# Kernel optimization log

Measured on AMD Instinct MI355X. Metric: run time of the kernel, lower is better.

## Reference

```python
import jax, jax.numpy as jnp
import numpy as np

HIDDEN = 1024
NUM_SLOTS = 8
VOCAB = 32768
B, T = 32, 2048


def setup_inputs() -> dict:
    key = jax.random.key(0)
    k1, k2, k3 = jax.random.split(key, 3)
    hidden_states = jax.random.normal(k1, (B, T, HIDDEN), dtype=jnp.float32)
    attention_mask = jnp.ones((B, T), dtype=jnp.int32)
    # slot projector weight, torch Linear stores [out, in] = [H*num_slots, H]
    W_proj = jax.random.normal(k2, (HIDDEN * NUM_SLOTS, HIDDEN), dtype=jnp.float32) * 0.02
    codebook = jax.random.normal(k3, (VOCAB, HIDDEN), dtype=jnp.float32) * 0.02
    return {"hidden_states": hidden_states, "attention_mask": attention_mask,
            "W_proj": W_proj, "codebook": codebook}


def _masked_mean(states, mask):
    # states [B,T,H], mask [B,T] -> [B,H]
    w = mask.astype(states.dtype)
    denom = jnp.clip(w.sum(axis=1, keepdims=True), 1.0)
    return jnp.einsum('bth,bt->bh', states, w) / denom


def reference(hidden_states, attention_mask, W_proj, codebook):
    pooled = _masked_mean(hidden_states, attention_mask)          # [B,H]
    pre_q = (pooled @ W_proj.T).reshape(-1, NUM_SLOTS, HIDDEN)    # [B,S,H]
    distances = (jnp.sum(pre_q ** 2, axis=-1, keepdims=True)
                 - 2.0 * jnp.einsum('bsh,vh->bsv', pre_q, codebook)
                 + jnp.sum(codebook ** 2, axis=-1)[None, None, :])  # [B,S,V]
    logits = -distances
    indices = jnp.argmax(logits, axis=-1)                         # [B,S]
    embedded = codebook[indices]                                  # [B,S,H]
    quantized = pre_q + jax.lax.stop_gradient(embedded - pre_q)
    commitment_loss = jnp.mean((pre_q - jax.lax.stop_gradient(embedded)) ** 2)
    codebook_loss = jnp.mean((embedded - jax.lax.stop_gradient(pre_q)) ** 2)
    return logits, indices, pre_q, quantized, commitment_loss, codebook_loss
```

## Files before the change

kernel.cpp:

```cpp
#include <hip/hip_runtime.h>
#include <hip/hip_bf16.h>

#define B_ 32
#define T_ 2048
#define H_ 1024
#define S_ 8
#define V_ 32768
#define ROWS 256
#define OUTO 8192
#define NCHUNK 64
#define TCHUNK 32
#define NCB 256
#define DELTA2 0.008f
#define MAXCAND 512

typedef __attribute__((ext_vector_type(8))) short s16x8;
typedef __attribute__((ext_vector_type(8))) unsigned short u16x8;
typedef __attribute__((ext_vector_type(4))) float f32x4;

__device__ __forceinline__ unsigned short bf16hi(float x) {
  return __builtin_bit_cast(unsigned short, __float2bfloat16(x));
}

__global__ void pool_kernel(const float* __restrict__ hidden,
                            const int* __restrict__ mask,
                            float* __restrict__ part_pool,
                            int* __restrict__ cntpart) {
  int b = blockIdx.x;
  int chunk = blockIdx.y;
  int t0 = chunk * TCHUNK;
  int h4 = threadIdx.x * 4;
  const float* base = hidden + ((size_t)b * T_ + t0) * H_ + h4;
  const int* mrow = mask + (size_t)b * T_ + t0;
  float a0 = 0.f, a1 = 0.f, a2 = 0.f, a3 = 0.f;
  int mcount = 0;
#pragma unroll 4
  for (int i = 0; i < TCHUNK; ++i) {
    int mi = mrow[i];
    float m = (float)mi;
    mcount += mi;
    float4 v = *reinterpret_cast<const float4*>(base + (size_t)i * H_);
    a0 += m * v.x; a1 += m * v.y; a2 += m * v.z; a3 += m * v.w;
  }
  float* pp = part_pool + ((size_t)chunk * B_ + b) * H_ + h4;
  *reinterpret_cast<float4*>(pp) = make_float4(a0, a1, a2, a3);
  if (threadIdx.x == 0) cntpart[chunk * B_ + b] = mcount;
}

__global__ void pool_reduce_kernel(const float* __restrict__ part_pool,
                                   const int* __restrict__ cntpart,
                                   float* __restrict__ pooledT,
                                   int* __restrict__ cnt) {
  int g = blockIdx.x * 256 + threadIdx.x;
  float s = 0.f;
  for (int c = 0; c < NCHUNK; ++c) s += part_pool[(size_t)c * (H_ * B_) + g];
  int b = g >> 10, h = g & 1023;
  pooledT[h * B_ + b] = s;
  if (g < B_) {
    int cs = 0;
    for (int c = 0; c < NCHUNK; ++c) cs += cntpart[c * B_ + g];
    cnt[g] = cs;
  }
}

__global__ __launch_bounds__(256) void proj_kernel(const float* __restrict__ Wp,
                            const float* __restrict__ pooledT,
                            const int* __restrict__ cnt,
                            float* __restrict__ preq) {
  __shared__ float pl[32][516];
  const int t = threadIdx.x;
  const int og = t >> 5, b = t & 31;
  const int o0 = blockIdx.x * 32;
  float acc0 = 0.f, acc1 = 0.f, acc2 = 0.f, acc3 = 0.f;
  const float* wb = Wp + (size_t)(o0 + og * 4) * H_;
  for (int pass = 0; pass < 2; ++pass) {
    int k0 = pass * 512;
    __syncthreads();
#pragma unroll
    for (int i = 0; i < 16; ++i) {
      int f = i * 1024 + t * 4;
      int hl = f >> 5, b4 = f & 31;
      float4 v = *reinterpret_cast<const float4*>(&pooledT[(size_t)(k0 + hl) * 32 + b4]);
      pl[b4 + 0][hl] = v.x; pl[b4 + 1][hl] = v.y;
      pl[b4 + 2][hl] = v.z; pl[b4 + 3][hl] = v.w;
    }
    __syncthreads();
    const float* w0 = wb + k0;
#pragma unroll 4
    for (int j = 0; j < 128; ++j) {
      float4 p = *reinterpret_cast<const float4*>(&pl[b][4 * j]);
      float4 a = *reinterpret_cast<const float4*>(w0 + 4 * j);
      float4 c = *reinterpret_cast<const float4*>(w0 + H_ + 4 * j);
      float4 d = *reinterpret_cast<const float4*>(w0 + 2 * H_ + 4 * j);
      float4 e = *reinterpret_cast<const float4*>(w0 + 3 * H_ + 4 * j);
      acc0 += a.x * p.x + a.y * p.y + a.z * p.z + a.w * p.w;
      acc1 += c.x * p.x + c.y * p.y + c.z * p.z + c.w * p.w;
      acc2 += d.x * p.x + d.y * p.y + d.z * p.z + d.w * p.w;
      acc3 += e.x * p.x + e.y * p.y + e.z * p.z + e.w * p.w;
    }
  }
  float denom = fmaxf((float)cnt[b], 1.0f);
  size_t obase = (size_t)b * OUTO + o0 + og * 4;
  preq[obase + 0] = acc0 / denom;
  preq[obase + 1] = acc1 / denom;
  preq[obase + 2] = acc2 / denom;
  preq[obase + 3] = acc3 / denom;
}

__global__ void aprep_kernel(const float* __restrict__ preq,
                             unsigned short* __restrict__ A_img,
                             float* __restrict__ xnorm) {
  int row = blockIdx.x;
  int t = threadIdx.x;
  int k0 = 4 * t;
  int ks = k0 >> 5, kk = k0 & 31;
  float4 v = reinterpret_cast<const float4*>(preq + (size_t)row * H_)[t];
  float xv[4] = {v.x, v.y, v.z, v.w};
  unsigned short hv[4];
  float s = 0.f;
#pragma unroll
  for (int i = 0; i < 4; ++i) { s += xv[i] * xv[i]; hv[i] = bf16hi(xv[i]); }
  *reinterpret_cast<ushort4*>(&A_img[(size_t)ks * 8192 + row * 32 + kk]) =
      make_ushort4(hv[0], hv[1], hv[2], hv[3]);
#pragma unroll
  for (int off = 1; off < 64; off <<= 1) s += __shfl_xor(s, off);
  __shared__ float ps[4];
  if ((t & 63) == 0) ps[t >> 6] = s;
  __syncthreads();
  if (t == 0) xnorm[row] = ps[0] + ps[1] + ps[2] + ps[3];
}

__global__ __launch_bounds__(512, 2) void dist_kernel(
    const unsigned short* __restrict__ A_img, const float* __restrict__ codebook,
    const float* __restrict__ xnorm, float* __restrict__ logits,
    float* __restrict__ pscore) {
  __shared__ __align__(16) unsigned short Bs[2][128][40];
  __shared__ float cn[128];
  __shared__ float xns[256];
  __shared__ float bwv[2][256];

  const int t = threadIdx.x;
  const int l = t & 63;
  const int w = t >> 6;
  const int cb = w & 1;
  const int m0 = (w >> 1) * 64;
  const int lr = l & 15, lq = l >> 4;
  const int blk = blockIdx.x;
  const int v0 = blk * 128;

  if (t < 256) xns[t] = xnorm[t];

  const int sn = t >> 2;
  const int sk = (t & 3) * 8;
  const float* cbp = codebook + (size_t)(v0 + sn) * H_ + sk;
  float csq = 0.f;

  f32x4 acc[4][4];
#pragma unroll
  for (int i = 0; i < 4; ++i)
#pragma unroll
    for (int j = 0; j < 4; ++j) acc[i][j] = (f32x4){0.f, 0.f, 0.f, 0.f};

  unsigned int aoff[4];
#pragma unroll
  for (int mt = 0; mt < 4; ++mt)
    aoff[mt] = (unsigned int)((m0 + mt * 16 + lr) * 32 + lq * 8);

#define LOAD_A(DST, KS)                                                           \
  _Pragma("unroll")                                                               \
  for (int mt = 0; mt < 4; ++mt)                                                  \
    DST[mt] = *reinterpret_cast<const s16x8*>(&A_img[(size_t)(KS) * 8192 + aoff[mt]]);

#define CONV(BUF, X0, X1)                                                         \
  {                                                                               \
    float xv[8] = {X0.x, X0.y, X0.z, X0.w, X1.x, X1.y, X1.z, X1.w};               \
    u16x8 hv;                                                                     \
    _Pragma("unroll")                                                             \
    for (int i = 0; i < 8; ++i) { float x = xv[i]; csq += x * x; hv[i] = bf16hi(x); } \
    *reinterpret_cast<u16x8*>(&Bs[BUF][sn][sk]) = hv;                             \
  }

#define BAR()                                                                     \
  asm volatile("s_waitcnt lgkmcnt(0)" ::: "memory");                              \
  __builtin_amdgcn_s_barrier();                                                   \
  __builtin_amdgcn_sched_barrier(0);

#define STEP(KS, AU, AN, CC0, CC1, CL0, CL1)                                      \
  {                                                                               \
    LOAD_A(AN, (KS) + 1);                                                         \
    int kl = (KS) + 3; if (kl > 31) kl = 31;                                      \
    CL0 = *reinterpret_cast<const float4*>(cbp + kl * 32);                        \
    CL1 = *reinterpret_cast<const float4*>(cbp + kl * 32 + 4);                    \
    s16x8 bh[4];                                                                  \
    _Pragma("unroll")                                                             \
    for (int nt = 0; nt < 4; ++nt)                                                \
      bh[nt] = *reinterpret_cast<const s16x8*>(&Bs[(KS) & 1][cb * 64 + nt * 16 + lr][lq * 8]); \
    __builtin_amdgcn_s_setprio(1);                                                \
    _Pragma("unroll")                                                             \
    for (int mt = 0; mt < 4; ++mt)                                                \
      _Pragma("unroll")                                                           \
      for (int nt = 0; nt < 4; ++nt)                                              \
        acc[mt][nt] = __builtin_amdgcn_mfma_f32_16x16x32_bf16(AU[mt], bh[nt], acc[mt][nt], 0, 0, 0); \
    __builtin_amdgcn_s_setprio(0);                                                \
    CONV(((KS) + 1) & 1, CC0, CC1);                                               \
    BAR();                                                                        \
  }

  s16x8 a0[4], a1[4], a2[4];
  LOAD_A(a0, 0);
  float4 c00 = *reinterpret_cast<const float4*>(cbp);
  float4 c01 = *reinterpret_cast<const float4*>(cbp + 4);
  float4 c10 = *reinterpret_cast<const float4*>(cbp + 32);
  float4 c11 = *reinterpret_cast<const float4*>(cbp + 36);
  float4 c20 = *reinterpret_cast<const float4*>(cbp + 64);
  float4 c21 = *reinterpret_cast<const float4*>(cbp + 68);
  CONV(0, c00, c01);
  BAR();

  for (int ks = 0; ks < 30; ks += 3) {
    STEP(ks,     a0, a1, c10, c11, c00, c01);
    STEP(ks + 1, a1, a2, c20, c21, c10, c11);
    STEP(ks + 2, a2, a0, c00, c01, c20, c21);
  }
  {
    LOAD_A(a1, 31);
    s16x8 bh[4];
#pragma unroll
    for (int nt = 0; nt < 4; ++nt)
      bh[nt] = *reinterpret_cast<const s16x8*>(&Bs[0][cb * 64 + nt * 16 + lr][lq * 8]);
    __builtin_amdgcn_s_setprio(1);
#pragma unroll
    for (int mt = 0; mt < 4; ++mt)
#pragma unroll
      for (int nt = 0; nt < 4; ++nt)
        acc[mt][nt] = __builtin_amdgcn_mfma_f32_16x16x32_bf16(a0[mt], bh[nt], acc[mt][nt], 0, 0, 0);
    __builtin_amdgcn_s_setprio(0);
    CONV(1, c10, c11);
    BAR();
  }
  {
    s16x8 bh[4];
#pragma unroll
    for (int nt = 0; nt < 4; ++nt)
      bh[nt] = *reinterpret_cast<const s16x8*>(&Bs[1][cb * 64 + nt * 16 + lr][lq * 8]);
    __builtin_amdgcn_s_setprio(1);
#pragma unroll
    for (int mt = 0; mt < 4; ++mt)
#pragma unroll
      for (int nt = 0; nt < 4; ++nt)
        acc[mt][nt] = __builtin_amdgcn_mfma_f32_16x16x32_bf16(a1[mt], bh[nt], acc[mt][nt], 0, 0, 0);
    __builtin_amdgcn_s_setprio(0);
  }

  csq += __shfl_xor(csq, 1);
  csq += __shfl_xor(csq, 2);
  if ((t & 3) == 0) cn[sn] = csq;
  __syncthreads();

  const float NEG = -3.402823466e38f;
#pragma unroll
  for (int mt = 0; mt < 4; ++mt) {
#pragma unroll
    for (int r = 0; r < 4; ++r) {
      int row = m0 + mt * 16 + lq * 4 + r;
      float xn = xns[row];
      float bs = NEG;
#pragma unroll
      for (int nt = 0; nt < 4; ++nt) {
        int col = cb * 64 + nt * 16 + lr;
        float sc = 2.f * acc[mt][nt][r] - cn[col];
        logits[(size_t)row * V_ + v0 + col] = sc - xn;
        bs = fmaxf(bs, sc);
      }
#pragma unroll
      for (int off = 1; off < 16; off <<= 1) bs = fmaxf(bs, __shfl_xor(bs, off));
      if (lr == 0) bwv[cb][row] = bs;
    }
  }
  __syncthreads();
  if (t < 256) pscore[(size_t)t * NCB + blk] = fmaxf(bwv[0][t], bwv[1][t]);
}

__global__ __launch_bounds__(256) void finalize_kernel(
    const float* __restrict__ preq, const float* __restrict__ codebook,
    const float* __restrict__ logits, const float* __restrict__ xnorm,
    const float* __restrict__ pscore,
    float* __restrict__ out_idx, float* __restrict__ out_quant,
    float* __restrict__ lsum) {
  int row = blockIdx.x;
  int t = threadIdx.x;
  float m = pscore[(size_t)row * NCB + t];
#pragma unroll
  for (int off = 1; off < 64; off <<= 1) m = fmaxf(m, __shfl_xor(m, off));
  __shared__ float wm[4];
  if ((t & 63) == 0) wm[t >> 6] = m;
  __syncthreads();
  float M = fmaxf(fmaxf(wm[0], wm[1]), fmaxf(wm[2], wm[3]));
  float thr = M - xnorm[row] - DELTA2;
  __shared__ int cand[MAXCAND];
  __shared__ int ncand;
  if (t == 0) ncand = 0;
  __syncthreads();
  const float* lrow = logits + (size_t)row * V_;
#pragma unroll 4
  for (int it = 0; it < 32; ++it) {
    int c0 = it * 1024 + t * 4;
    float4 lg = *reinterpret_cast<const float4*>(lrow + c0);
    if (lg.x >= thr) { int p = atomicAdd(&ncand, 1); if (p < MAXCAND) cand[p] = c0; }
    if (lg.y >= thr) { int p = atomicAdd(&ncand, 1); if (p < MAXCAND) cand[p] = c0 + 1; }
    if (lg.z >= thr) { int p = atomicAdd(&ncand, 1); if (p < MAXCAND) cand[p] = c0 + 2; }
    if (lg.w >= thr) { int p = atomicAdd(&ncand, 1); if (p < MAXCAND) cand[p] = c0 + 3; }
  }
  __syncthreads();
  int total = ncand;
  const float* pr = preq + (size_t)row * H_;
  int idx;
  if (total <= MAXCAND) {
    __shared__ double sd[4];
    double best = -1.0e300; int bi = V_;
    for (int j = 0; j < total; ++j) {
      int c = cand[j];
      const float* cr = codebook + (size_t)c * H_;
      float4 cv = reinterpret_cast<const float4*>(cr)[t];
      float4 pv = reinterpret_cast<const float4*>(pr)[t];
      double p = (double)cv.x * (2.0 * (double)pv.x - (double)cv.x)
               + (double)cv.y * (2.0 * (double)pv.y - (double)cv.y)
               + (double)cv.z * (2.0 * (double)pv.z - (double)cv.z)
               + (double)cv.w * (2.0 * (double)pv.w - (double)cv.w);
#pragma unroll
      for (int off = 1; off < 64; off <<= 1) p += __shfl_xor(p, off);
      if ((t & 63) == 0) sd[t >> 6] = p;
      __syncthreads();
      double s = sd[0] + sd[1] + sd[2] + sd[3];
      if (s > best || (s == best && c < bi)) { best = s; bi = c; }
      __syncthreads();
    }
    idx = bi;
  } else {
    double best = -1.0e300; int bi = V_;
    for (int c = t; c < V_; c += 256) {
      const float* cr = codebook + (size_t)c * H_;
      double s = 0.0;
      for (int k = 0; k < H_; k += 4) {
        float4 cv = *reinterpret_cast<const float4*>(cr + k);
        float4 pv = *reinterpret_cast<const float4*>(pr + k);
        s += (double)cv.x * (2.0 * (double)pv.x - (double)cv.x)
           + (double)cv.y * (2.0 * (double)pv.y - (double)cv.y)
           + (double)cv.z * (2.0 * (double)pv.z - (double)cv.z)
           + (double)cv.w * (2.0 * (double)pv.w - (double)cv.w);
      }
      if (s > best || (s == best && c < bi)) { best = s; bi = c; }
    }
#pragma unroll
    for (int off = 1; off < 64; off <<= 1) {
      double os = __shfl_xor(best, off);
      int oi = __shfl_xor(bi, off);
      if (os > best || (os == best && oi < bi)) { best = os; bi = oi; }
    }
    __shared__ double fb[4]; __shared__ int fbi[4];
    if ((t & 63) == 0) { fb[t >> 6] = best; fbi[t >> 6] = bi; }
    __syncthreads();
    double b0 = fb[0]; int i0 = fbi[0];
    for (int wv = 1; wv < 4; ++wv)
      if (fb[wv] > b0 || (fb[wv] == b0 && fbi[wv] < i0)) { b0 = fb[wv]; i0 = fbi[wv]; }
    idx = i0;
  }
  if (t == 0) out_idx[row] = (float)idx;
  float4 e = reinterpret_cast<const float4*>(codebook + (size_t)idx * H_)[t];
  float4 p4 = reinterpret_cast<const float4*>(pr)[t];
  float4 q;
  q.x = p4.x + (e.x - p4.x); q.y = p4.y + (e.y - p4.y);
  q.z = p4.z + (e.z - p4.z); q.w = p4.w + (e.w - p4.w);
  reinterpret_cast<float4*>(out_quant)[row * 256 + t] = q;
  float dx = p4.x - e.x, dy = p4.y - e.y, dz = p4.z - e.z, dw = p4.w - e.w;
  float ls = dx * dx + dy * dy + dz * dz + dw * dw;
#pragma unroll
  for (int off = 1; off < 64; off <<= 1) ls += __shfl_xor(ls, off);
  __shared__ float lss[4];
  if ((t & 63) == 0) lss[t >> 6] = ls;
  __syncthreads();
  if (t == 0) lsum[row] = lss[0] + lss[1] + lss[2] + lss[3];
}

__global__ void loss_kernel(const float* __restrict__ lsum, float* __restrict__ out_loss) {
  int t = threadIdx.x;
  float s = lsum[t];
#pragma unroll
  for (int off = 1; off < 64; off <<= 1) s += __shfl_xor(s, off);
  __shared__ float a[4];
  if ((t & 63) == 0) a[t >> 6] = s;
  __syncthreads();
  if (t == 0) {
    float lv = (a[0] + a[1] + a[2] + a[3]) / (float)(ROWS * H_);
    out_loss[0] = lv; out_loss[1] = lv;
  }
}

extern "C" void kernel_launch(void* const* d_in, const int* in_sizes, int n_in,
                              void* d_out, int out_size, void* d_ws, size_t ws_size,
                              hipStream_t stream) {
  (void)in_sizes; (void)n_in; (void)out_size; (void)ws_size;
  const float* hidden   = (const float*)d_in[0];
  const int* mask       = (const int*)d_in[1];
  const float* Wp       = (const float*)d_in[2];
  const float* codebook = (const float*)d_in[3];

  float* out = (float*)d_out;
  float* out_logits = out;
  float* out_idx    = out + 8388608;
  float* out_preq   = out_idx + 256;
  float* out_quant  = out_preq + 262144;
  float* out_loss   = out_quant + 262144;

  float* part_pool = out_logits;
  int*   cntpart   = (int*)(out_logits + 2097152);
  float* pooledT   = out_logits + 2099200;
  int*   cnt       = (int*)(out_logits + 2131968);

  float* ws     = (float*)d_ws;
  float* xnorm  = ws;
  float* pscore = ws + 256;
  float* lsum   = ws + 65792;
  unsigned short* A_img = (unsigned short*)(ws + 66048);

  pool_kernel<<<dim3(B_, NCHUNK), 256, 0, stream>>>(hidden, mask, part_pool, cntpart);
  pool_reduce_kernel<<<128, 256, 0, stream>>>(part_pool, cntpart, pooledT, cnt);
  proj_kernel<<<256, 256, 0, stream>>>(Wp, pooledT, cnt, out_preq);
  aprep_kernel<<<ROWS, 256, 0, stream>>>(out_preq, A_img, xnorm);
  dist_kernel<<<NCB, 512, 0, stream>>>(A_img, codebook, xnorm, out_logits, pscore);
  finalize_kernel<<<ROWS, 256, 0, stream>>>(out_preq, codebook, out_logits, xnorm,
                                            pscore, out_idx, out_quant, lsum);
  loss_kernel<<<1, 256, 0, stream>>>(lsum, out_loss);
}
```

Measured before the change: 197.4 us.

## Fuse aprep into proj epilogue and loss into finalize via atomic ticket

The bf16 A-image packing and row-norm computation move into the projection kernel's epilogue, using atomicAdd to accumulate xnorm, which is now zeroed in pool_reduce. The loss reduction folds into finalize through a last-block ticket counter. The pooling kernel uses larger time chunks with four independent load streams for more memory-level parallelism. Together these remove two kernel launches and one pass over pre_q, at the cost of atomic contention on xnorm and a done counter that is never reset but is handled by a modulo-256 check.

```diff
diff --git a/kernel.cpp b/kernel.cpp
--- a/kernel.cpp
+++ b/kernel.cpp
@@ -8,8 +8,8 @@
 #define V_ 32768
 #define ROWS 256
 #define OUTO 8192
-#define NCHUNK 64
-#define TCHUNK 32
+#define NCHUNK 32
+#define TCHUNK 64
 #define NCB 256
 #define DELTA2 0.008f
 #define MAXCAND 512
@@ -35,12 +35,21 @@
   float a0 = 0.f, a1 = 0.f, a2 = 0.f, a3 = 0.f;
   int mcount = 0;
 #pragma unroll 4
-  for (int i = 0; i < TCHUNK; ++i) {
-    int mi = mrow[i];
-    float m = (float)mi;
-    mcount += mi;
-    float4 v = *reinterpret_cast<const float4*>(base + (size_t)i * H_);
-    a0 += m * v.x; a1 += m * v.y; a2 += m * v.z; a3 += m * v.w;
+  for (int i = 0; i < 16; ++i) {
+    int mi0 = mrow[i];
+    int mi1 = mrow[i + 16];
+    int mi2 = mrow[i + 32];
+    int mi3 = mrow[i + 48];
+    float4 v0 = *reinterpret_cast<const float4*>(base + (size_t)i * H_);
+    float4 v1 = *reinterpret_cast<const float4*>(base + (size_t)(i + 16) * H_);
+    float4 v2 = *reinterpret_cast<const float4*>(base + (size_t)(i + 32) * H_);
+    float4 v3 = *reinterpret_cast<const float4*>(base + (size_t)(i + 48) * H_);
+    mcount += mi0 + mi1 + mi2 + mi3;
+    float f0 = (float)mi0, f1 = (float)mi1, f2 = (float)mi2, f3 = (float)mi3;
+    a0 += f0 * v0.x + f1 * v1.x + f2 * v2.x + f3 * v3.x;
+    a1 += f0 * v0.y + f1 * v1.y + f2 * v2.y + f3 * v3.y;
+    a2 += f0 * v0.z + f1 * v1.z + f2 * v2.z + f3 * v3.z;
+    a3 += f0 * v0.w + f1 * v1.w + f2 * v2.w + f3 * v3.w;
   }
   float* pp = part_pool + ((size_t)chunk * B_ + b) * H_ + h4;
   *reinterpret_cast<float4*>(pp) = make_float4(a0, a1, a2, a3);
@@ -50,12 +59,14 @@
 __global__ void pool_reduce_kernel(const float* __restrict__ part_pool,
                                    const int* __restrict__ cntpart,
                                    float* __restrict__ pooledT,
-                                   int* __restrict__ cnt) {
+                                   int* __restrict__ cnt,
+                                   float* __restrict__ xnorm) {
   int g = blockIdx.x * 256 + threadIdx.x;
   float s = 0.f;
   for (int c = 0; c < NCHUNK; ++c) s += part_pool[(size_t)c * (H_ * B_) + g];
   int b = g >> 10, h = g & 1023;
   pooledT[h * B_ + b] = s;
+  if (g < ROWS) xnorm[g] = 0.f;
   if (g < B_) {
     int cs = 0;
     for (int c = 0; c < NCHUNK; ++c) cs += cntpart[c * B_ + g];
@@ -66,8 +77,10 @@
 __global__ __launch_bounds__(256) void proj_kernel(const float* __restrict__ Wp,
                             const float* __restrict__ pooledT,
                             const int* __restrict__ cnt,
-                            float* __restrict__ preq) {
-  __shared__ float pl[32][516];
+                            float* __restrict__ preq,
+                            unsigned short* __restrict__ A_img,
+                            float* __restrict__ xnorm) {
+  __shared__ float pl[32][520];
   const int t = threadIdx.x;
   const int og = t >> 5, b = t & 31;
   const int o0 = blockIdx.x * 32;
@@ -100,34 +113,19 @@
     }
   }
   float denom = fmaxf((float)cnt[b], 1.0f);
+  float v0 = acc0 / denom, v1 = acc1 / denom, v2 = acc2 / denom, v3 = acc3 / denom;
   size_t obase = (size_t)b * OUTO + o0 + og * 4;
-  preq[obase + 0] = acc0 / denom;
-  preq[obase + 1] = acc1 / denom;
-  preq[obase + 2] = acc2 / denom;
-  preq[obase + 3] = acc3 / denom;
-}
-
-__global__ void aprep_kernel(const float* __restrict__ preq,
-                             unsigned short* __restrict__ A_img,
-                             float* __restrict__ xnorm) {
-  int row = blockIdx.x;
-  int t = threadIdx.x;
-  int k0 = 4 * t;
-  int ks = k0 >> 5, kk = k0 & 31;
-  float4 v = reinterpret_cast<const float4*>(preq + (size_t)row * H_)[t];
-  float xv[4] = {v.x, v.y, v.z, v.w};
-  unsigned short hv[4];
-  float s = 0.f;
-#pragma unroll
-  for (int i = 0; i < 4; ++i) { s += xv[i] * xv[i]; hv[i] = bf16hi(xv[i]); }
-  *reinterpret_cast<ushort4*>(&A_img[(size_t)ks * 8192 + row * 32 + kk]) =
-      make_ushort4(hv[0], hv[1], hv[2], hv[3]);
-#pragma unroll
-  for (int off = 1; off < 64; off <<= 1) s += __shfl_xor(s, off);
-  __shared__ float ps[4];
-  if ((t & 63) == 0) ps[t >> 6] = s;
-  __syncthreads();
-  if (t == 0) xnorm[row] = ps[0] + ps[1] + ps[2] + ps[3];
+  preq[obase + 0] = v0;
+  preq[obase + 1] = v1;
+  preq[obase + 2] = v2;
+  preq[obase + 3] = v3;
+  int o = o0 + og * 4;
+  int srow = b * 8 + (o >> 10);
+  int h = o & 1023;
+  int ks = h >> 5, kk = h & 31;
+  *reinterpret_cast<ushort4*>(&A_img[(size_t)ks * 8192 + srow * 32 + kk]) =
+      make_ushort4(bf16hi(v0), bf16hi(v1), bf16hi(v2), bf16hi(v3));
+  atomicAdd(&xnorm[srow], v0 * v0 + v1 * v1 + v2 * v2 + v3 * v3);
 }
 
 __global__ __launch_bounds__(512, 2) void dist_kernel(
@@ -286,7 +284,8 @@
     const float* __restrict__ logits, const float* __restrict__ xnorm,
     const float* __restrict__ pscore,
     float* __restrict__ out_idx, float* __restrict__ out_quant,
-    float* __restrict__ lsum) {
+    float* __restrict__ lsum, unsigned int* __restrict__ done_ctr,
+    float* __restrict__ out_loss) {
   int row = blockIdx.x;
   int t = threadIdx.x;
   float m = pscore[(size_t)row * NCB + t];
@@ -380,19 +379,25 @@
   if ((t & 63) == 0) lss[t >> 6] = ls;
   __syncthreads();
   if (t == 0) lsum[row] = lss[0] + lss[1] + lss[2] + lss[3];
-}
-
-__global__ void loss_kernel(const float* __restrict__ lsum, float* __restrict__ out_loss) {
-  int t = threadIdx.x;
-  float s = lsum[t];
-#pragma unroll
-  for (int off = 1; off < 64; off <<= 1) s += __shfl_xor(s, off);
-  __shared__ float a[4];
-  if ((t & 63) == 0) a[t >> 6] = s;
-  __syncthreads();
+
+  __shared__ unsigned int tkt;
   if (t == 0) {
-    float lv = (a[0] + a[1] + a[2] + a[3]) / (float)(ROWS * H_);
-    out_loss[0] = lv; out_loss[1] = lv;
+    __threadfence();
+    tkt = __hip_atomic_fetch_add(done_ctr, 1u, __ATOMIC_ACQ_REL, __HIP_MEMORY_SCOPE_AGENT);
+  }
+  __syncthreads();
+  if ((tkt & 255u) == 255u) {
+    __threadfence();
+    float s = __hip_atomic_load(&lsum[t], __ATOMIC_RELAXED, __HIP_MEMORY_SCOPE_AGENT);
+#pragma unroll
+    for (int off = 1; off < 64; off <<= 1) s += __shfl_xor(s, off);
+    __shared__ float la[4];
+    if ((t & 63) == 0) la[t >> 6] = s;
+    __syncthreads();
+    if (t == 0) {
+      float lv = (la[0] + la[1] + la[2] + la[3]) / (float)(ROWS * H_);
+      out_loss[0] = lv; out_loss[1] = lv;
+    }
   }
 }
 
@@ -413,22 +418,22 @@
   float* out_loss   = out_quant + 262144;
 
   float* part_pool = out_logits;
-  int*   cntpart   = (int*)(out_logits + 2097152);
-  float* pooledT   = out_logits + 2099200;
-  int*   cnt       = (int*)(out_logits + 2131968);
+  int*   cntpart   = (int*)(out_logits + 1048576);
+  float* pooledT   = out_logits + 1049600;
+  int*   cnt       = (int*)(out_logits + 1082368);
 
   float* ws     = (float*)d_ws;
   float* xnorm  = ws;
   float* pscore = ws + 256;
   float* lsum   = ws + 65792;
-  unsigned short* A_img = (unsigned short*)(ws + 66048);
+  unsigned int* done_ctr = (unsigned int*)(ws + 66048);
+  unsigned short* A_img = (unsigned short*)(ws + 66052);
 
   pool_kernel<<<dim3(B_, NCHUNK), 256, 0, stream>>>(hidden, mask, part_pool, cntpart);
-  pool_reduce_kernel<<<128, 256, 0, stream>>>(part_pool, cntpart, pooledT, cnt);
-  proj_kernel<<<256, 256, 0, stream>>>(Wp, pooledT, cnt, out_preq);
-  aprep_kernel<<<ROWS, 256, 0, stream>>>(out_preq, A_img, xnorm);
+  pool_reduce_kernel<<<128, 256, 0, stream>>>(part_pool, cntpart, pooledT, cnt, xnorm);
+  proj_kernel<<<256, 256, 0, stream>>>(Wp, pooledT, cnt, out_preq, A_img, xnorm);
   dist_kernel<<<NCB, 512, 0, stream>>>(A_img, codebook, xnorm, out_logits, pscore);
   finalize_kernel<<<ROWS, 256, 0, stream>>>(out_preq, codebook, out_logits, xnorm,
-                                            pscore, out_idx, out_quant, lsum);
-  loss_kernel<<<1, 256, 0, stream>>>(lsum, out_loss);
-}
+                                            pscore, out_idx, out_quant, lsum,
+                                            done_ctr, out_loss);
+}
```

Result: slower. 247.0 us (+25.1%).
